# Performance work log

Hardware: AMD Instinct MI355X
Metric: run time of the kernel (lower is better)

Reference implementation:

```python
import jax, jax.numpy as jnp
import numpy as np
from jax import lax

V, E, H, C = 50000, 300, 300, 3
TP, TH, B = 128, 64, 256


def _cell(x, h, c, Wih, Whh, bih, bhh):
    # PyTorch LSTMCell: gate order i, f, g, o
    g = x @ Wih.T + bih + h @ Whh.T + bhh
    i, f, gg, o = jnp.split(g, 4, axis=-1)
    c2 = jax.nn.sigmoid(f) * c + jax.nn.sigmoid(i) * jnp.tanh(gg)
    return jax.nn.sigmoid(o) * jnp.tanh(c2), c2


def setup_inputs() -> dict:
    key = jax.random.key(0)
    ks = iter(jax.random.split(key, 32))
    def n(shape, s=0.05):
        return jax.random.normal(next(ks), shape, dtype=jnp.float32) * s
    return {
        "premise": jax.random.randint(next(ks), (TP, B), 0, V),
        "premise_len": jax.random.randint(next(ks), (B,), 1, TP),
        "hypothesis": jax.random.randint(next(ks), (TH, B), 0, V),
        "hypothesis_len": jax.random.randint(next(ks), (B,), 1, TH),
        "word2vec": n((V, E), 1.0),
        "w_e": jax.random.uniform(next(ks), (H,), dtype=jnp.float32),
        "W_s": n((H, H)), "W_t": n((H, H)), "W_m": n((H, H)),
        "fc_w": n((C, H)), "fc_b": n((C,)),
        "prem_Wih": n((4 * H, E)), "prem_Whh": n((4 * H, H)),
        "prem_bih": n((4 * H,)), "prem_bhh": n((4 * H,)),
        "hypo_Wih": n((4 * H, E)), "hypo_Whh": n((4 * H, H)),
        "hypo_bih": n((4 * H,)), "hypo_bhh": n((4 * H,)),
        "match_Wih": n((4 * H, 2 * H)), "match_Whh": n((4 * H, H)),
        "match_bih": n((4 * H,)), "match_bhh": n((4 * H,)),
    }


def reference(premise, premise_len, hypothesis, hypothesis_len, word2vec,
              w_e, W_s, W_t, W_m, fc_w, fc_b,
              prem_Wih, prem_Whh, prem_bih, prem_bhh,
              hypo_Wih, hypo_Whh, hypo_bih, hypo_bhh,
              match_Wih, match_Whh, match_bih, match_bhh):
    b = premise.shape[1]
    h = w_e.shape[0]
    prem_e = word2vec[premise]      # [TP, B, E]
    hypo_e = word2vec[hypothesis]   # [TH, B, E]
    z = jnp.zeros((b, h), dtype=word2vec.dtype)

    # premise LSTM over time
    def prem_step(carry, x):
        hs, cs = carry
        hs, cs = _cell(x, hs, cs, prem_Wih, prem_Whh, prem_bih, prem_bhh)
        return (hs, cs), hs
    _, h_s = lax.scan(prem_step, (z, z), prem_e)  # [TP, B, H]

    # precompute W_s @ h_s (invariant across hypothesis steps)
    ws_hs = jnp.einsum('tbh,kh->tbk', h_s, W_s)   # [TP, B, H]

    # hypothesis LSTM + per-step tanh attention + match cell (zero hx each step,
    # matching the original call lstm_match(m_k) with no hx)
    def hypo_step(carry, x):
        h_t, c_t, h_m = carry
        h_t, c_t = _cell(x, h_t, c_t, hypo_Wih, hypo_Whh, hypo_bih, hypo_bhh)
        q = h_t @ W_t.T + h_m @ W_m.T                   # [B, H]
        s = jnp.tanh(ws_hs + q[None])                   # [TP, B, H]
        e = jnp.einsum('tbh,h->tb', s, w_e)             # [TP, B]
        alpha = jax.nn.softmax(e, axis=0)               # softmax over premise positions
        a = jnp.einsum('tb,tbh->bh', alpha, h_s)        # [B, H]
        m = jnp.concatenate([a, h_t], axis=1)           # [B, 2H]
        h_m_new, _ = _cell(m, z, z, match_Wih, match_Whh, match_bih, match_bhh)
        return (h_t, c_t, h_m_new), None

    (_, _, h_m), _ = lax.scan(hypo_step, (z, z, z), hypo_e)
    return h_m @ fc_w.T + fc_b  # [B, C]
```

## Files before the change

kernel.cpp:

```cpp
#include <hip/hip_runtime.h>
#include <hip/hip_bf16.h>
#include <cstddef>

#define HDIM 300
#define EDIM 300
#define BATCH 256
#define TPREM 128
#define THYP 64
#define KTT 32

typedef unsigned short us8 __attribute__((ext_vector_type(8)));

__device__ __forceinline__ float fast_sigm(float x) {
    return 1.f / (1.f + __expf(-x));
}
__device__ __forceinline__ float fast_tanh(float x) {
    float e = __expf(2.f * x);
    return 1.f - 2.f / (e + 1.f);
}
__device__ __forceinline__ unsigned short f2bf(float f) {
    __hip_bfloat16 h = __float2bfloat16(f);
    return *reinterpret_cast<unsigned short*>(&h);
}
__device__ __forceinline__ float bf2f(unsigned short u) {
    return __uint_as_float((unsigned)u << 16);
}

struct Params {
    const int* premise; const int* hypothesis;
    const float* w2v; const float* w_e;
    const float* W_s; const float* W_t; const float* W_m;
    const float* fc_w; const float* fc_b;
    const float* pWih; const float* pWhh; const float* pbih; const float* pbhh;
    const float* hWih; const float* hWhh; const float* hbih; const float* hbhh;
    const float* mWih; const float* mbih; const float* mbhh;
    float* h_t_all;
    unsigned short* hsT;
    unsigned short* wshsT;
    unsigned short* wthtB;
    unsigned short* Xp;
    unsigned short* Xh;
    unsigned short* WhhW_p;
    unsigned short* WhhW_h;
    unsigned short* WmW3;
    unsigned short* WmTw;
    float* out;
};

__global__ void k_init(Params p) {
    const int stride = gridDim.x * 256;
    const int i0 = blockIdx.x * 256 + threadIdx.x;
    for (int i = i0; i < 38 * 1536 * 8; i += stride) {
        int kg = i / (1536 * 8);
        int rem = i - kg * (1536 * 8);
        int c = rem >> 3, j = rem & 7;
        int k = 8 * kg + j;
        float vp = 0.f, vh = 0.f;
        if (c < 1200 && k < 300) {
            vp = p.pWhh[(size_t)c * 300 + k];
            vh = p.hWhh[(size_t)c * 300 + k];
        }
        p.WhhW_p[i] = f2bf(vp);
        p.WhhW_h[i] = f2bf(vh);
    }
    for (int i = i0; i < 75 * 1024 * 8; i += stride) {
        int kg = i / (1024 * 8);
        int rem = i - kg * (1024 * 8);
        int c = rem >> 3, j = rem & 7;
        int k = 8 * kg + j;
        float v = 0.f;
        if (c < 900 && k < 600) {
            int row = c + (c < 300 ? 0 : 300);
            v = p.mWih[(size_t)row * 600 + k];
        }
        p.WmW3[i] = f2bf(v);
    }
    for (int i = i0; i < 38 * 304 * 8; i += stride) {
        int kg = i / (304 * 8);
        int rem = i - kg * (304 * 8);
        int c = rem >> 3, j = rem & 7;
        int k = 8 * kg + j;
        p.WmTw[i] = f2bf((c < 300 && k < 300) ? p.W_m[(size_t)c * 300 + k] : 0.f);
    }
}

__global__ __launch_bounds__(256, 2) void k_xproj(Params p) {
    __shared__ __align__(16) float As[16][136];
    __shared__ __align__(16) float Bs[16][68];
    __shared__ int toks[128];

    const int bid = blockIdx.x;
    const int mt = bid / 19, nt = bid % 19;
    const bool isP = mt < 256;
    const int m0 = (isP ? mt : mt - 256) * 128;
    const int n0 = nt * 64;
    const int* tk = isP ? p.premise : p.hypothesis;
    const float* W = isP ? p.pWih : p.hWih;
    const float* b1 = isP ? p.pbih : p.hbih;
    const float* b2 = isP ? p.pbhh : p.hbhh;
    unsigned short* X = isP ? p.Xp : p.Xh;
    const int tid = threadIdx.x;

    if (tid < 128) toks[tid] = tk[m0 + tid];
    __syncthreads();

    const int tm = tid & 15, tn = tid >> 4;
    float acc[8][4] = {};
    for (int k0 = 0; k0 < 300; k0 += 16) {
        for (int i = tid; i < 2048; i += 256) {
            int kk = i & 15, ml = i >> 4;
            int k = k0 + kk;
            As[kk][ml] = (k < 300)
                ? p.w2v[(size_t)toks[ml] * 300 + k] : 0.f;
        }
        for (int i = tid; i < 1024; i += 256) {
            int kk = i & 15, nl = i >> 4;
            int c = n0 + nl, k = k0 + kk;
            Bs[kk][nl] = (c < 1200 && k < 300)
                ? W[(size_t)c * 300 + k] : 0.f;
        }
        __syncthreads();
        #pragma unroll
        for (int kk = 0; kk < 16; ++kk) {
            float a[8], w[4];
            #pragma unroll
            for (int i = 0; i < 8; ++i) a[i] = As[kk][tm * 8 + i];
            #pragma unroll
            for (int j = 0; j < 4; ++j) w[j] = Bs[kk][tn * 4 + j];
            #pragma unroll
            for (int i = 0; i < 8; ++i)
                #pragma unroll
                for (int j = 0; j < 4; ++j)
                    acc[i][j] = fmaf(a[i], w[j], acc[i][j]);
        }
        __syncthreads();
    }
    #pragma unroll
    for (int i = 0; i < 8; ++i) {
        int rr = m0 + tm * 8 + i;
        int t = rr >> 8, b = rr & 255;
        int g = b >> 2, r = b & 3;
        size_t base = (size_t)(t * 64 + g) * 1200;
        #pragma unroll
        for (int j = 0; j < 4; ++j) {
            int c = n0 + tn * 4 + j;
            if (c < 1200)
                X[(base + c) * 4 + r] = f2bf(acc[i][j] + b1[c] + b2[c]);
        }
    }
}

__global__ __launch_bounds__(512, 2) void match_b(Params p) {
    __shared__ __align__(16) float4 A[304];
    __shared__ __align__(16) float4 G[1536];

    const int blk = blockIdx.x;
    const int tid = threadIdx.x;
    const bool isP = blk < 64;
    const int g = isP ? blk : blk - 64;
    const int b0 = g * 4;
    const int TS = isP ? TPREM : THYP;
    const unsigned short* WhhW = isP ? p.WhhW_p : p.WhhW_h;
    const unsigned short* Xbuf = isP ? p.Xp : p.Xh;

    if (tid < 304) A[tid] = {0, 0, 0, 0};
    float4 creg = {0, 0, 0, 0};
    __syncthreads();

    for (int t = 0; t < TS; ++t) {
        float4 ac0 = {0,0,0,0}, ac1 = {0,0,0,0}, ac2 = {0,0,0,0};
        {
            const unsigned short* w0 = WhhW + (size_t)tid * 8;
            const unsigned short* w1 = WhhW + (size_t)(tid + 512) * 8;
            const unsigned short* w2 = WhhW + (size_t)(tid + 1024) * 8;
            for (int kg = 0; kg < 38; kg += 2) {
                const size_t offA = (size_t)kg * (1536 * 8);
                const size_t offB = (size_t)(kg + 1) * (1536 * 8);
                us8 u0a = *reinterpret_cast<const us8*>(w0 + offA);
                us8 u1a = *reinterpret_cast<const us8*>(w1 + offA);
                us8 u2a = *reinterpret_cast<const us8*>(w2 + offA);
                us8 u0b = *reinterpret_cast<const us8*>(w0 + offB);
                us8 u1b = *reinterpret_cast<const us8*>(w1 + offB);
                us8 u2b = *reinterpret_cast<const us8*>(w2 + offB);
                #pragma unroll
                for (int j = 0; j < 8; ++j) {
                    float4 a = A[8 * kg + j];
                    float f0 = bf2f(u0a[j]), f1 = bf2f(u1a[j]), f2 = bf2f(u2a[j]);
                    ac0.x = fmaf(a.x, f0, ac0.x); ac0.y = fmaf(a.y, f0, ac0.y);
                    ac0.z = fmaf(a.z, f0, ac0.z); ac0.w = fmaf(a.w, f0, ac0.w);
                    ac1.x = fmaf(a.x, f1, ac1.x); ac1.y = fmaf(a.y, f1, ac1.y);
                    ac1.z = fmaf(a.z, f1, ac1.z); ac1.w = fmaf(a.w, f1, ac1.w);
                    ac2.x = fmaf(a.x, f2, ac2.x); ac2.y = fmaf(a.y, f2, ac2.y);
                    ac2.z = fmaf(a.z, f2, ac2.z); ac2.w = fmaf(a.w, f2, ac2.w);
                }
                #pragma unroll
                for (int j = 0; j < 8; ++j) {
                    float4 a = A[8 * (kg + 1) + j];
                    float f0 = bf2f(u0b[j]), f1 = bf2f(u1b[j]), f2 = bf2f(u2b[j]);
                    ac0.x = fmaf(a.x, f0, ac0.x); ac0.y = fmaf(a.y, f0, ac0.y);
                    ac0.z = fmaf(a.z, f0, ac0.z); ac0.w = fmaf(a.w, f0, ac0.w);
                    ac1.x = fmaf(a.x, f1, ac1.x); ac1.y = fmaf(a.y, f1, ac1.y);
                    ac1.z = fmaf(a.z, f1, ac1.z); ac1.w = fmaf(a.w, f1, ac1.w);
                    ac2.x = fmaf(a.x, f2, ac2.x); ac2.y = fmaf(a.y, f2, ac2.y);
                    ac2.z = fmaf(a.z, f2, ac2.z); ac2.w = fmaf(a.w, f2, ac2.w);
                }
            }
        }
        G[tid] = ac0;
        G[tid + 512] = ac1;
        G[tid + 1024] = ac2;
        __syncthreads();

        if (tid < 300) {
            const unsigned short* xb = Xbuf + (size_t)(t * 64 + g) * 1200 * 4;
            ushort4 xi = *reinterpret_cast<const ushort4*>(xb + (size_t)tid * 4);
            ushort4 xf = *reinterpret_cast<const ushort4*>(xb + (size_t)(tid + 300) * 4);
            ushort4 xg = *reinterpret_cast<const ushort4*>(xb + (size_t)(tid + 600) * 4);
            ushort4 xo = *reinterpret_cast<const ushort4*>(xb + (size_t)(tid + 900) * 4);
            float4 g_i = G[tid], g_f = G[300 + tid];
            float4 g_g = G[600 + tid], g_o = G[900 + tid];
            float4 h4;
            {
                float gi = fast_sigm(g_i.x + bf2f(xi.x));
                float gf = fast_sigm(g_f.x + bf2f(xf.x));
                float gg = fast_tanh(g_g.x + bf2f(xg.x));
                float go = fast_sigm(g_o.x + bf2f(xo.x));
                creg.x = gf * creg.x + gi * gg; h4.x = go * fast_tanh(creg.x);
            }
            {
                float gi = fast_sigm(g_i.y + bf2f(xi.y));
                float gf = fast_sigm(g_f.y + bf2f(xf.y));
                float gg = fast_tanh(g_g.y + bf2f(xg.y));
                float go = fast_sigm(g_o.y + bf2f(xo.y));
                creg.y = gf * creg.y + gi * gg; h4.y = go * fast_tanh(creg.y);
            }
            {
                float gi = fast_sigm(g_i.z + bf2f(xi.z));
                float gf = fast_sigm(g_f.z + bf2f(xf.z));
                float gg = fast_tanh(g_g.z + bf2f(xg.z));
                float go = fast_sigm(g_o.z + bf2f(xo.z));
                creg.z = gf * creg.z + gi * gg; h4.z = go * fast_tanh(creg.z);
            }
            {
                float gi = fast_sigm(g_i.w + bf2f(xi.w));
                float gf = fast_sigm(g_f.w + bf2f(xf.w));
                float gg = fast_tanh(g_g.w + bf2f(xg.w));
                float go = fast_sigm(g_o.w + bf2f(xo.w));
                creg.w = gf * creg.w + gi * gg; h4.w = go * fast_tanh(creg.w);
            }
            A[tid] = h4;
            if (isP) {
                p.hsT[((size_t)(b0 + 0) * TPREM + t) * HDIM + tid] = f2bf(h4.x);
                p.hsT[((size_t)(b0 + 1) * TPREM + t) * HDIM + tid] = f2bf(h4.y);
                p.hsT[((size_t)(b0 + 2) * TPREM + t) * HDIM + tid] = f2bf(h4.z);
                p.hsT[((size_t)(b0 + 3) * TPREM + t) * HDIM + tid] = f2bf(h4.w);
            } else {
                const size_t rb = (size_t)(t * BATCH + b0);
                p.h_t_all[(rb + 0) * HDIM + tid] = h4.x;
                p.h_t_all[(rb + 1) * HDIM + tid] = h4.y;
                p.h_t_all[(rb + 2) * HDIM + tid] = h4.z;
                p.h_t_all[(rb + 3) * HDIM + tid] = h4.w;
            }
        }
        __syncthreads();
    }
}

__global__ __launch_bounds__(256, 2) void k_proj(Params p) {
    __shared__ __align__(16) float hA[320][34];
    __shared__ __align__(16) float Bs[KTT][68];

    const int jb = blockIdx.x;
    const int tid = threadIdx.x;
    const int pb = tid & 15, hl = tid >> 4;
    const bool isP = jb < 1024;
    const int rt = isP ? jb : jb - 1024;
    const float* Wp = isP ? p.W_s : p.W_t;
    const int fb_c = tid >> 2, fb_k0 = (tid & 3) * 8;

    for (int i2 = tid; i2 < 32 * HDIM; i2 += 256) {
        int r = i2 / HDIM, k = i2 - r * HDIM;
        hA[k][r] = isP
            ? bf2f(p.hsT[(size_t)(rt * 32 + r) * HDIM + k])
            : p.h_t_all[(size_t)(rt * 32 + r) * HDIM + k];
    }
    for (int i2 = tid; i2 < 20 * 34; i2 += 256)
        hA[300 + i2 / 34][i2 % 34] = 0.f;
    __syncthreads();

    unsigned short* dst = isP ? p.wshsT : p.wthtB;

    for (int n0 = 0; n0 < HDIM; n0 += 64) {
        const int wrow = n0 + fb_c;
        const bool wvalid = wrow < HDIM;
        float acc[2][4] = {};
        for (int kc = 0; kc < HDIM; kc += KTT) {
            #pragma unroll
            for (int u = 0; u < 8; ++u) {
                int kk = fb_k0 + u, k = kc + kk;
                Bs[kk][fb_c] = (wvalid && k < HDIM)
                    ? Wp[(size_t)wrow * HDIM + k] : 0.f;
            }
            __syncthreads();
            #pragma unroll
            for (int kk = 0; kk < KTT; ++kk) {
                float2 av = *(const float2*)&hA[kc + kk][pb * 2];
                float4 wv = *(const float4*)&Bs[kk][hl * 4];
                acc[0][0] = fmaf(av.x, wv.x, acc[0][0]);
                acc[0][1] = fmaf(av.x, wv.y, acc[0][1]);
                acc[0][2] = fmaf(av.x, wv.z, acc[0][2]);
                acc[0][3] = fmaf(av.x, wv.w, acc[0][3]);
                acc[1][0] = fmaf(av.y, wv.x, acc[1][0]);
                acc[1][1] = fmaf(av.y, wv.y, acc[1][1]);
                acc[1][2] = fmaf(av.y, wv.z, acc[1][2]);
                acc[1][3] = fmaf(av.y, wv.w, acc[1][3]);
            }
            __syncthreads();
        }
        const int col = n0 + hl * 4;
        if (col < HDIM) {
            #pragma unroll
            for (int u = 0; u < 2; ++u) {
                size_t rr = (size_t)(rt * 32 + pb * 2 + u);
                ushort4 v4;
                v4.x = f2bf(acc[u][0]); v4.y = f2bf(acc[u][1]);
                v4.z = f2bf(acc[u][2]); v4.w = f2bf(acc[u][3]);
                *reinterpret_cast<ushort4*>(&dst[rr * HDIM + col]) = v4;
            }
        }
        __syncthreads();
    }
}

__global__ __launch_bounds__(1024, 1) void match_d(Params p) {
    __shared__ __align__(16) float hm[304];
    __shared__ __align__(16) float q[304];
    __shared__ __align__(16) float we[304];
    __shared__ float alpha[TPREM];
    __shared__ __align__(16) float A6[608];
    __shared__ float G[1024];
    __shared__ __align__(16) float pvp[16][304];

    const int b = blockIdx.x;
    const int tid = threadIdx.x;
    const int lane = tid & 63;
    const int wv = tid >> 6;
    const unsigned short* wsb = p.wshsT + (size_t)b * TPREM * HDIM;
    const unsigned short* hsb = p.hsT + (size_t)b * TPREM * HDIM;

    float bi0 = 0.f, bi2 = 0.f, bi3 = 0.f;
    if (tid < 304) { hm[tid] = 0.f; we[tid] = 0.f; q[tid] = 0.f; }
    if (tid >= 600 && tid < 608) A6[tid] = 0.f;
    if (tid < 300) {
        we[tid] = p.w_e[tid];
        bi0 = p.mbih[tid] + p.mbhh[tid];
        bi2 = p.mbih[600 + tid] + p.mbhh[600 + tid];
        bi3 = p.mbih[900 + tid] + p.mbhh[900 + tid];
    }
    __syncthreads();

    for (int k = 0; k < THYP; ++k) {
        if (tid < 304) {
            float acc = 0.f;
            const unsigned short* w0 = p.WmTw + (size_t)tid * 8;
            for (int kg = 0; kg < 38; kg += 2) {
                us8 ua = *reinterpret_cast<const us8*>(w0 + (size_t)kg * (304 * 8));
                us8 ub = *reinterpret_cast<const us8*>(w0 + (size_t)(kg + 1) * (304 * 8));
                #pragma unroll
                for (int j = 0; j < 8; ++j)
                    acc = fmaf(hm[8 * kg + j], bf2f(ua[j]), acc);
                #pragma unroll
                for (int j = 0; j < 8; ++j)
                    acc = fmaf(hm[8 * (kg + 1) + j], bf2f(ub[j]), acc);
            }
            if (tid < 300)
                q[tid] = acc + bf2f(p.wthtB[((size_t)k * BATCH + b) * HDIM + tid]);
        }
        __syncthreads();

        for (int t = wv; t < TPREM; t += 16) {
            const unsigned short* row = wsb + (size_t)t * HDIM;
            ushort4 v4 = *reinterpret_cast<const ushort4*>(&row[4 * lane]);
            float4 q4 = *reinterpret_cast<const float4*>(&q[4 * lane]);
            float4 we4 = *reinterpret_cast<const float4*>(&we[4 * lane]);
            float pp;
            pp  = we4.x * fast_tanh(bf2f(v4.x) + q4.x);
            pp += we4.y * fast_tanh(bf2f(v4.y) + q4.y);
            pp += we4.z * fast_tanh(bf2f(v4.z) + q4.z);
            pp += we4.w * fast_tanh(bf2f(v4.w) + q4.w);
            if (lane < 44) {
                int h = 256 + lane;
                pp += we[h] * fast_tanh(bf2f(row[h]) + q[h]);
            }
            #pragma unroll
            for (int off = 32; off; off >>= 1) pp += __shfl_xor(pp, off, 64);
            if (lane == 0) alpha[t] = pp;
        }
        __syncthreads();

        if (wv == 0) {
            float e0 = alpha[lane], e1 = alpha[64 + lane];
            float m = fmaxf(e0, e1);
            #pragma unroll
            for (int off = 32; off; off >>= 1) m = fmaxf(m, __shfl_xor(m, off, 64));
            e0 = __expf(e0 - m); e1 = __expf(e1 - m);
            float s = e0 + e1;
            #pragma unroll
            for (int off = 32; off; off >>= 1) s += __shfl_xor(s, off, 64);
            float inv = 1.f / s;
            alpha[lane] = e0 * inv;
            alpha[64 + lane] = e1 * inv;
        }
        __syncthreads();

        {
            float4 acc = {0, 0, 0, 0};
            float at = 0.f;
            for (int t = wv; t < TPREM; t += 16) {
                float wgt = alpha[t];
                const unsigned short* row = hsb + (size_t)t * HDIM;
                ushort4 v4 = *reinterpret_cast<const ushort4*>(&row[4 * lane]);
                acc.x = fmaf(wgt, bf2f(v4.x), acc.x);
                acc.y = fmaf(wgt, bf2f(v4.y), acc.y);
                acc.z = fmaf(wgt, bf2f(v4.z), acc.z);
                acc.w = fmaf(wgt, bf2f(v4.w), acc.w);
                if (lane < 44) at = fmaf(wgt, bf2f(row[256 + lane]), at);
            }
            *reinterpret_cast<float4*>(&pvp[wv][4 * lane]) = acc;
            if (lane < 44) pvp[wv][256 + lane] = at;
        }
        __syncthreads();

        if (tid < 300) {
            float s = 0.f;
            #pragma unroll
            for (int w16 = 0; w16 < 16; ++w16) s += pvp[w16][tid];
            A6[tid] = s;
            A6[300 + tid] = p.h_t_all[((size_t)k * BATCH + b) * HDIM + tid];
        }
        __syncthreads();

        {
            float acc0 = 0.f;
            const unsigned short* w0 = p.WmW3 + (size_t)tid * 8;
            for (int kb = 0; kb < 75; kb += 5) {
                us8 u0 = *reinterpret_cast<const us8*>(w0 + (size_t)(kb + 0) * (1024 * 8));
                us8 u1 = *reinterpret_cast<const us8*>(w0 + (size_t)(kb + 1) * (1024 * 8));
                us8 u2 = *reinterpret_cast<const us8*>(w0 + (size_t)(kb + 2) * (1024 * 8));
                us8 u3 = *reinterpret_cast<const us8*>(w0 + (size_t)(kb + 3) * (1024 * 8));
                us8 u4 = *reinterpret_cast<const us8*>(w0 + (size_t)(kb + 4) * (1024 * 8));
                #pragma unroll
                for (int j = 0; j < 8; ++j)
                    acc0 = fmaf(A6[8 * (kb + 0) + j], bf2f(u0[j]), acc0);
                #pragma unroll
                for (int j = 0; j < 8; ++j)
                    acc0 = fmaf(A6[8 * (kb + 1) + j], bf2f(u1[j]), acc0);
                #pragma unroll
                for (int j = 0; j < 8; ++j)
                    acc0 = fmaf(A6[8 * (kb + 2) + j], bf2f(u2[j]), acc0);
                #pragma unroll
                for (int j = 0; j < 8; ++j)
                    acc0 = fmaf(A6[8 * (kb + 3) + j], bf2f(u3[j]), acc0);
                #pragma unroll
                for (int j = 0; j < 8; ++j)
                    acc0 = fmaf(A6[8 * (kb + 4) + j], bf2f(u4[j]), acc0);
            }
            G[tid] = acc0;
        }
        __syncthreads();

        if (tid < 300) {
            float gi = fast_sigm(G[tid] + bi0);
            float gg = fast_tanh(G[300 + tid] + bi2);
            float go = fast_sigm(G[600 + tid] + bi3);
            hm[tid] = go * fast_tanh(gi * gg);
        }
        __syncthreads();
    }

    if (wv == 0) {
        float p0 = 0.f, p1 = 0.f, p2 = 0.f;
        #pragma unroll
        for (int i = 0; i < 5; ++i) {
            int h = lane + 64 * i;
            if (h < HDIM) {
                float v = hm[h];
                p0 = fmaf(v, p.fc_w[h], p0);
                p1 = fmaf(v, p.fc_w[HDIM + h], p1);
                p2 = fmaf(v, p.fc_w[2 * HDIM + h], p2);
            }
        }
        #pragma unroll
        for (int off = 32; off; off >>= 1) {
            p0 += __shfl_xor(p0, off, 64);
            p1 += __shfl_xor(p1, off, 64);
            p2 += __shfl_xor(p2, off, 64);
        }
        if (lane == 0) {
            p.out[b * 3 + 0] = p0 + p.fc_b[0];
            p.out[b * 3 + 1] = p1 + p.fc_b[1];
            p.out[b * 3 + 2] = p2 + p.fc_b[2];
        }
    }
}

__global__ void k_lstm_gates(
    const int* __restrict__ tok, const float* __restrict__ w2v,
    const float* __restrict__ A0, int K0,
    const float* __restrict__ A1, int K1,
    const float* __restrict__ W0, int ld0,
    const float* __restrict__ W1, int ld1,
    const float* __restrict__ bih, const float* __restrict__ bhh,
    const float* __restrict__ c_in, float* __restrict__ c_out,
    float* __restrict__ h_out)
{
    constexpr int KT = 32;
    __shared__ __align__(16) float As[KT][34];
    __shared__ __align__(16) float Bs[KT][68];

    const int tid = threadIdx.x;
    const int b0 = blockIdx.x * 32;
    const int hh0 = blockIdx.y * 16;
    const int K = K0 + K1;
    const int pb = tid & 15;
    const int hl = tid >> 4;
    const int fa_b = tid >> 3;
    const int fa_k0 = (tid & 7) * 4;
    const int fb_c = tid >> 2;
    const int fb_k0 = (tid & 3) * 8;
    const int fb_hh = hh0 + (fb_c >> 2);
    const int fb_g = fb_c & 3;
    const int fb_row = fb_g * HDIM + fb_hh;
    const bool fb_valid = fb_hh < HDIM;
    const int ga = b0 + fa_b;
    const int tok_b = tok ? tok[ga] : 0;

    float acc[2][4] = {{0.f,0.f,0.f,0.f},{0.f,0.f,0.f,0.f}};

    for (int k0 = 0; k0 < K; k0 += KT) {
        #pragma unroll
        for (int u = 0; u < 4; ++u) {
            int kk = fa_k0 + u;
            int k = k0 + kk;
            float v = 0.f;
            if (k < K0)      v = tok ? w2v[(size_t)tok_b * K0 + k]
                                     : A0[(size_t)ga * K0 + k];
            else if (k < K)  v = A1[(size_t)ga * K1 + (k - K0)];
            As[kk][fa_b] = v;
        }
        #pragma unroll
        for (int u = 0; u < 8; ++u) {
            int kk = fb_k0 + u;
            int k = k0 + kk;
            float v = 0.f;
            if (fb_valid) {
                if (k < K0)     v = W0[(size_t)fb_row * ld0 + k];
                else if (k < K) v = W1[(size_t)fb_row * ld1 + (k - K0)];
            }
            Bs[kk][fb_c] = v;
        }
        __syncthreads();
        #pragma unroll
        for (int kk = 0; kk < KT; ++kk) {
            float2 av = *(const float2*)&As[kk][pb * 2];
            float4 wv = *(const float4*)&Bs[kk][hl * 4];
            acc[0][0] = fmaf(av.x, wv.x, acc[0][0]);
            acc[0][1] = fmaf(av.x, wv.y, acc[0][1]);
            acc[0][2] = fmaf(av.x, wv.z, acc[0][2]);
            acc[0][3] = fmaf(av.x, wv.w, acc[0][3]);
            acc[1][0] = fmaf(av.y, wv.x, acc[1][0]);
            acc[1][1] = fmaf(av.y, wv.y, acc[1][1]);
            acc[1][2] = fmaf(av.y, wv.z, acc[1][2]);
            acc[1][3] = fmaf(av.y, wv.w, acc[1][3]);
        }
        __syncthreads();
    }

    const int hh = hh0 + hl;
    if (hh < HDIM) {
        float bi = bih[hh] + bhh[hh];
        float bf = bih[HDIM + hh] + bhh[HDIM + hh];
        float bg = bih[2 * HDIM + hh] + bhh[2 * HDIM + hh];
        float bo = bih[3 * HDIM + hh] + bhh[3 * HDIM + hh];
        #pragma unroll
        for (int u = 0; u < 2; ++u) {
            int b = b0 + pb * 2 + u;
            float gi = fast_sigm(acc[u][0] + bi);
            float gf = fast_sigm(acc[u][1] + bf);
            float gg = fast_tanh(acc[u][2] + bg);
            float go = fast_sigm(acc[u][3] + bo);
            float c = gf * c_in[(size_t)b * HDIM + hh] + gi * gg;
            c_out[(size_t)b * HDIM + hh] = c;
            h_out[(size_t)b * HDIM + hh] = go * fast_tanh(c);
        }
    }
}

template<int BM, int BN, int TM, int TN, int KT>
__global__ void k_gemm_tn(
    const float* __restrict__ A0, int K0,
    const float* __restrict__ A1, int K1,
    const float* __restrict__ B0, int ldb0,
    const float* __restrict__ B1, int ldb1,
    float* __restrict__ C, int M, int N)
{
    __shared__ __align__(16) float As[KT][BM + 4];
    __shared__ __align__(16) float Bs[KT][BN + 4];
    const int tid = threadIdx.x;
    const int m0 = blockIdx.x * BM;
    const int n0 = blockIdx.y * BN;
    const int K = K0 + K1;
    constexpr int TPM = BM / TM;
    const int tm = tid % TPM;
    const int tn = tid / TPM;

    float acc[TM][TN];
    #pragma unroll
    for (int i = 0; i < TM; ++i)
        #pragma unroll
        for (int j = 0; j < TN; ++j) acc[i][j] = 0.f;

    for (int k0 = 0; k0 < K; k0 += KT) {
        for (int i = tid; i < KT * BM; i += 256) {
            int kk = i % KT, ml = i / KT;
            int m = m0 + ml, k = k0 + kk;
            float v = 0.f;
            if (m < M) {
                if (k < K0)     v = A0[(size_t)m * K0 + k];
                else if (k < K) v = A1[(size_t)m * K1 + (k - K0)];
            }
            As[kk][ml] = v;
        }
        for (int i = tid; i < KT * BN; i += 256) {
            int kk = i % KT, nl = i / KT;
            int n = n0 + nl, k = k0 + kk;
            float v = 0.f;
            if (n < N) {
                if (k < K0)     v = B0[(size_t)n * ldb0 + k];
                else if (k < K) v = B1[(size_t)n * ldb1 + (k - K0)];
            }
            Bs[kk][nl] = v;
        }
        __syncthreads();
        #pragma unroll
        for (int kk = 0; kk < KT; ++kk) {
            float a[TM], w[TN];
            #pragma unroll
            for (int i = 0; i < TM; ++i) a[i] = As[kk][tm * TM + i];
            #pragma unroll
            for (int j = 0; j < TN; ++j) w[j] = Bs[kk][tn * TN + j];
            #pragma unroll
            for (int i = 0; i < TM; ++i)
                #pragma unroll
                for (int j = 0; j < TN; ++j)
                    acc[i][j] = fmaf(a[i], w[j], acc[i][j]);
        }
        __syncthreads();
    }
    #pragma unroll
    for (int i = 0; i < TM; ++i) {
        int m = m0 + tm * TM + i;
        if (m >= M) continue;
        #pragma unroll
        for (int j = 0; j < TN; ++j) {
            int n = n0 + tn * TN + j;
            if (n < N) C[(size_t)m * N + n] = acc[i][j];
        }
    }
}

__global__ void k_attn(const float* __restrict__ ws_hs,
                       const float* __restrict__ h_s,
                       const float* __restrict__ q,
                       const float* __restrict__ w_e,
                       float* __restrict__ a_out)
{
    const int b = blockIdx.x;
    const int tid = threadIdx.x;
    const int lane = tid & 63;
    const int wv = tid >> 6;

    __shared__ float q_s[HDIM];
    __shared__ float we_s[HDIM];
    __shared__ float alpha[TPREM];
    __shared__ float red[4];

    for (int h = tid; h < HDIM; h += 256) {
        q_s[h] = q[(size_t)b * HDIM + h];
        we_s[h] = w_e[h];
    }
    __syncthreads();

    for (int t = wv; t < TPREM; t += 4) {
        const float* row = ws_hs + ((size_t)t * BATCH + b) * HDIM;
        float p = 0.f;
        for (int h = lane; h < HDIM; h += 64)
            p += we_s[h] * fast_tanh(row[h] + q_s[h]);
        #pragma unroll
        for (int off = 32; off; off >>= 1) p += __shfl_xor(p, off, 64);
        if (lane == 0) alpha[t] = p;
    }
    __syncthreads();

    if (wv < 2) {
        float ev = alpha[tid];
        float m = ev;
        #pragma unroll
        for (int off = 32; off; off >>= 1) m = fmaxf(m, __shfl_xor(m, off, 64));
        if (lane == 0) red[wv] = m;
        __syncthreads();
        float gm = fmaxf(red[0], red[1]);
        float e = __expf(ev - gm);
        alpha[tid] = e;
        float s = e;
        #pragma unroll
        for (int off = 32; off; off >>= 1) s += __shfl_xor(s, off, 64);
        if (lane == 0) red[2 + wv] = s;
        __syncthreads();
        alpha[tid] *= 1.f / (red[2] + red[3]);
    } else {
        __syncthreads();
        __syncthreads();
    }
    __syncthreads();

    for (int h = tid; h < HDIM; h += 256) {
        const float* hsb = h_s + (size_t)b * HDIM + h;
        float acc = 0.f;
        #pragma unroll 4
        for (int t = 0; t < TPREM; ++t)
            acc = fmaf(alpha[t], hsb[(size_t)t * BATCH * HDIM], acc);
        a_out[(size_t)b * HDIM + h] = acc;
    }
}

__global__ void k_fc(const float* __restrict__ h_m,
                     const float* __restrict__ fc_w,
                     const float* __restrict__ fc_b,
                     float* __restrict__ out)
{
    const int b = threadIdx.x;
    float a0 = 0.f, a1 = 0.f, a2 = 0.f;
    for (int h = 0; h < HDIM; ++h) {
        float v = h_m[(size_t)b * HDIM + h];
        a0 = fmaf(v, fc_w[h], a0);
        a1 = fmaf(v, fc_w[HDIM + h], a1);
        a2 = fmaf(v, fc_w[2 * HDIM + h], a2);
    }
    out[b * 3 + 0] = a0 + fc_b[0];
    out[b * 3 + 1] = a1 + fc_b[1];
    out[b * 3 + 2] = a2 + fc_b[2];
}

extern "C" void kernel_launch(void* const* d_in, const int* in_sizes, int n_in,
                              void* d_out, int out_size, void* d_ws, size_t ws_size,
                              hipStream_t stream) {
    (void)in_sizes; (void)n_in; (void)out_size;
    const int*   premise    = (const int*)d_in[0];
    const int*   hypothesis = (const int*)d_in[2];
    const float* w2v        = (const float*)d_in[4];
    const float* w_e        = (const float*)d_in[5];
    const float* W_s        = (const float*)d_in[6];
    const float* W_t        = (const float*)d_in[7];
    const float* W_m        = (const float*)d_in[8];
    const float* fc_w       = (const float*)d_in[9];
    const float* fc_b       = (const float*)d_in[10];
    const float* pWih       = (const float*)d_in[11];
    const float* pWhh       = (const float*)d_in[12];
    const float* pbih       = (const float*)d_in[13];
    const float* pbhh       = (const float*)d_in[14];
    const float* hWih       = (const float*)d_in[15];
    const float* hWhh       = (const float*)d_in[16];
    const float* hbih       = (const float*)d_in[17];
    const float* hbhh       = (const float*)d_in[18];
    const float* mWih       = (const float*)d_in[19];
    const float* mbih       = (const float*)d_in[21];
    const float* mbhh       = (const float*)d_in[22];

    const size_t BH = (size_t)BATCH * HDIM;
    const size_t F32_CNT = (size_t)THYP * BH;
    const size_t NWHH = (size_t)38 * 1536 * 8;
    const size_t NWM3 = (size_t)75 * 1024 * 8;
    const size_t NWMT = (size_t)38 * 304 * 8;
    const size_t U16_CNT = 2 * (size_t)TPREM * BH
                         + (size_t)THYP * BH
                         + (size_t)TPREM * 64 * 1200 * 4
                         + (size_t)THYP * 64 * 1200 * 4
                         + 2 * NWHH + NWM3 + NWMT;
    const size_t NEED = F32_CNT * 4 + U16_CNT * 2 + 256;

    if (ws_size >= NEED) {
        Params p;
        p.premise = premise; p.hypothesis = hypothesis;
        p.w2v = w2v; p.w_e = w_e;
        p.W_s = W_s; p.W_t = W_t; p.W_m = W_m;
        p.fc_w = fc_w; p.fc_b = fc_b;
        p.pWih = pWih; p.pWhh = pWhh; p.pbih = pbih; p.pbhh = pbhh;
        p.hWih = hWih; p.hWhh = hWhh; p.hbih = hbih; p.hbhh = hbhh;
        p.mWih = mWih; p.mbih = mbih; p.mbhh = mbhh;

        float* f = (float*)d_ws;
        p.h_t_all = f; f += F32_CNT;
        unsigned short* u = (unsigned short*)f;
        p.hsT    = u; u += (size_t)TPREM * BH;
        p.wshsT  = u; u += (size_t)TPREM * BH;
        p.wthtB  = u; u += (size_t)THYP * BH;
        p.Xp     = u; u += (size_t)TPREM * 64 * 1200 * 4;
        p.Xh     = u; u += (size_t)THYP * 64 * 1200 * 4;
        p.WhhW_p = u; u += NWHH;
        p.WhhW_h = u; u += NWHH;
        p.WmW3   = u; u += NWM3;
        p.WmTw   = u;
        p.out = (float*)d_out;

        k_init<<<512, 256, 0, stream>>>(p);
        k_xproj<<<(256 + 128) * 19, 256, 0, stream>>>(p);
        match_b<<<128, 512, 0, stream>>>(p);
        k_proj<<<1536, 256, 0, stream>>>(p);
        match_d<<<BATCH, 1024, 0, stream>>>(p);
        return;
    }

    float* ws    = (float*)d_ws;
    float* h_s   = ws;
    float* wshs  = h_s + (size_t)TPREM * BH;
    float* zeros = wshs + (size_t)TPREM * BH;
    float* c_p   = zeros + BH;
    float* c_h   = c_p + BH;
    float* c_m   = c_h + BH;
    float* ht0   = c_m + BH;
    float* ht1   = ht0 + BH;
    float* h_m   = ht1 + BH;
    float* qb    = h_m + BH;
    float* ab    = qb + BH;

    (void)hipMemsetAsync(zeros, 0, BH * sizeof(float), stream);
    (void)hipMemsetAsync(c_p,   0, BH * sizeof(float), stream);
    (void)hipMemsetAsync(c_h,   0, BH * sizeof(float), stream);
    (void)hipMemsetAsync(h_m,   0, BH * sizeof(float), stream);

    dim3 gGate(BATCH / 32, (HDIM + 15) / 16);

    for (int t = 0; t < TPREM; ++t) {
        const float* hp = t ? (h_s + (size_t)(t - 1) * BH) : zeros;
        k_lstm_gates<<<gGate, 256, 0, stream>>>(
            premise + (size_t)t * BATCH, w2v, nullptr, EDIM,
            hp, HDIM, pWih, EDIM, pWhh, HDIM,
            pbih, pbhh, c_p, c_p, h_s + (size_t)t * BH);
    }

    k_gemm_tn<64, 64, 4, 4, 16><<<dim3(TPREM * BATCH / 64, (HDIM + 63) / 64), 256, 0, stream>>>(
        h_s, HDIM, nullptr, 0, W_s, HDIM, nullptr, 0, wshs, TPREM * BATCH, HDIM);

    for (int k = 0; k < THYP; ++k) {
        const float* hp = k ? ((k & 1) ? ht0 : ht1) : zeros;
        float* hc = (k & 1) ? ht1 : ht0;
        k_lstm_gates<<<gGate, 256, 0, stream>>>(
            hypothesis + (size_t)k * BATCH, w2v, nullptr, EDIM,
            hp, HDIM, hWih, EDIM, hWhh, HDIM,
            hbih, hbhh, c_h, c_h, hc);
        k_gemm_tn<16, 64, 1, 4, 16><<<dim3(BATCH / 16, (HDIM + 63) / 64), 256, 0, stream>>>(
            hc, HDIM, h_m, HDIM, W_t, HDIM, W_m, HDIM, qb, BATCH, HDIM);
        k_attn<<<BATCH, 256, 0, stream>>>(wshs, h_s, qb, w_e, ab);
        k_lstm_gates<<<gGate, 256, 0, stream>>>(
            nullptr, nullptr, ab, HDIM,
            hc, HDIM, mWih, 2 * HDIM, mWih + HDIM, 2 * HDIM,
            mbih, mbhh, zeros, c_m, h_m);
    }

    k_fc<<<1, BATCH, 0, stream>>>(h_m, fc_w, fc_b, (float*)d_out);
}
```

Before: 4.820 ms.

## Halve batch per block in LSTM recurrence and split-K the attention query GEMV

The premise and hypothesis LSTM recurrence kernel now processes 2 batch columns per block instead of 4, doubling the grid to 256 blocks so more CUs work on the sequential recurrence. The cost is that each block re-reads the full recurrent weight matrix, so weight traffic doubles. Separately, the per-step W_m·h_m GEMV in the match kernel is split across 912 threads in three K-chunks that are reduced through shared memory, in place of only 304 active threads. That adds an extra barrier each hypothesis step.

```diff
diff --git a/kernel.cpp b/kernel.cpp
--- a/kernel.cpp
+++ b/kernel.cpp
@@ -151,24 +151,26 @@
 }
 
 __global__ __launch_bounds__(512, 2) void match_b(Params p) {
-    __shared__ __align__(16) float4 A[304];
-    __shared__ __align__(16) float4 G[1536];
+    __shared__ __align__(16) float2 A[304];
+    __shared__ __align__(16) float2 G[1536];
 
     const int blk = blockIdx.x;
     const int tid = threadIdx.x;
-    const bool isP = blk < 64;
-    const int g = isP ? blk : blk - 64;
-    const int b0 = g * 4;
+    const bool isP = blk < 128;
+    const int g = isP ? blk : blk - 128;
+    const int b0 = g * 2;
     const int TS = isP ? TPREM : THYP;
     const unsigned short* WhhW = isP ? p.WhhW_p : p.WhhW_h;
     const unsigned short* Xbuf = isP ? p.Xp : p.Xh;
-
-    if (tid < 304) A[tid] = {0, 0, 0, 0};
-    float4 creg = {0, 0, 0, 0};
+    const int g4 = b0 >> 2;
+    const int r0 = b0 & 3;
+
+    if (tid < 304) A[tid] = {0, 0};
+    float2 creg = {0, 0};
     __syncthreads();
 
     for (int t = 0; t < TS; ++t) {
-        float4 ac0 = {0,0,0,0}, ac1 = {0,0,0,0}, ac2 = {0,0,0,0};
+        float2 ac0 = {0,0}, ac1 = {0,0}, ac2 = {0,0};
         {
             const unsigned short* w0 = WhhW + (size_t)tid * 8;
             const unsigned short* w1 = WhhW + (size_t)(tid + 512) * 8;
@@ -184,25 +186,19 @@
                 us8 u2b = *reinterpret_cast<const us8*>(w2 + offB);
                 #pragma unroll
                 for (int j = 0; j < 8; ++j) {
-                    float4 a = A[8 * kg + j];
+                    float2 a = A[8 * kg + j];
                     float f0 = bf2f(u0a[j]), f1 = bf2f(u1a[j]), f2 = bf2f(u2a[j]);
                     ac0.x = fmaf(a.x, f0, ac0.x); ac0.y = fmaf(a.y, f0, ac0.y);
-                    ac0.z = fmaf(a.z, f0, ac0.z); ac0.w = fmaf(a.w, f0, ac0.w);
                     ac1.x = fmaf(a.x, f1, ac1.x); ac1.y = fmaf(a.y, f1, ac1.y);
-                    ac1.z = fmaf(a.z, f1, ac1.z); ac1.w = fmaf(a.w, f1, ac1.w);
                     ac2.x = fmaf(a.x, f2, ac2.x); ac2.y = fmaf(a.y, f2, ac2.y);
-                    ac2.z = fmaf(a.z, f2, ac2.z); ac2.w = fmaf(a.w, f2, ac2.w);
                 }
                 #pragma unroll
                 for (int j = 0; j < 8; ++j) {
-                    float4 a = A[8 * (kg + 1) + j];
+                    float2 a = A[8 * (kg + 1) + j];
                     float f0 = bf2f(u0b[j]), f1 = bf2f(u1b[j]), f2 = bf2f(u2b[j]);
                     ac0.x = fmaf(a.x, f0, ac0.x); ac0.y = fmaf(a.y, f0, ac0.y);
-                    ac0.z = fmaf(a.z, f0, ac0.z); ac0.w = fmaf(a.w, f0, ac0.w);
                     ac1.x = fmaf(a.x, f1, ac1.x); ac1.y = fmaf(a.y, f1, ac1.y);
-                    ac1.z = fmaf(a.z, f1, ac1.z); ac1.w = fmaf(a.w, f1, ac1.w);
                     ac2.x = fmaf(a.x, f2, ac2.x); ac2.y = fmaf(a.y, f2, ac2.y);
-                    ac2.z = fmaf(a.z, f2, ac2.z); ac2.w = fmaf(a.w, f2, ac2.w);
                 }
             }
         }
@@ -212,54 +208,36 @@
         __syncthreads();
 
         if (tid < 300) {
-            const unsigned short* xb = Xbuf + (size_t)(t * 64 + g) * 1200 * 4;
-            ushort4 xi = *reinterpret_cast<const ushort4*>(xb + (size_t)tid * 4);
-            ushort4 xf = *reinterpret_cast<const ushort4*>(xb + (size_t)(tid + 300) * 4);
-            ushort4 xg = *reinterpret_cast<const ushort4*>(xb + (size_t)(tid + 600) * 4);
-            ushort4 xo = *reinterpret_cast<const ushort4*>(xb + (size_t)(tid + 900) * 4);
-            float4 g_i = G[tid], g_f = G[300 + tid];
-            float4 g_g = G[600 + tid], g_o = G[900 + tid];
-            float4 h4;
+            const unsigned short* xb = Xbuf + (size_t)(t * 64 + g4) * 1200 * 4 + r0;
+            ushort2 xi = *reinterpret_cast<const ushort2*>(xb + (size_t)tid * 4);
+            ushort2 xf = *reinterpret_cast<const ushort2*>(xb + (size_t)(tid + 300) * 4);
+            ushort2 xg = *reinterpret_cast<const ushort2*>(xb + (size_t)(tid + 600) * 4);
+            ushort2 xo = *reinterpret_cast<const ushort2*>(xb + (size_t)(tid + 900) * 4);
+            float2 g_i = G[tid], g_f = G[300 + tid];
+            float2 g_g = G[600 + tid], g_o = G[900 + tid];
+            float2 h2;
             {
                 float gi = fast_sigm(g_i.x + bf2f(xi.x));
                 float gf = fast_sigm(g_f.x + bf2f(xf.x));
                 float gg = fast_tanh(g_g.x + bf2f(xg.x));
                 float go = fast_sigm(g_o.x + bf2f(xo.x));
-                creg.x = gf * creg.x + gi * gg; h4.x = go * fast_tanh(creg.x);
+                creg.x = gf * creg.x + gi * gg; h2.x = go * fast_tanh(creg.x);
             }
             {
                 float gi = fast_sigm(g_i.y + bf2f(xi.y));
                 float gf = fast_sigm(g_f.y + bf2f(xf.y));
                 float gg = fast_tanh(g_g.y + bf2f(xg.y));
                 float go = fast_sigm(g_o.y + bf2f(xo.y));
-                creg.y = gf * creg.y + gi * gg; h4.y = go * fast_tanh(creg.y);
-            }
-            {
-                float gi = fast_sigm(g_i.z + bf2f(xi.z));
-                float gf = fast_sigm(g_f.z + bf2f(xf.z));
-                float gg = fast_tanh(g_g.z + bf2f(xg.z));
-                float go = fast_sigm(g_o.z + bf2f(xo.z));
-                creg.z = gf * creg.z + gi * gg; h4.z = go * fast_tanh(creg.z);
-            }
-            {
-                float gi = fast_sigm(g_i.w + bf2f(xi.w));
-                float gf = fast_sigm(g_f.w + bf2f(xf.w));
-                float gg = fast_tanh(g_g.w + bf2f(xg.w));
-                float go = fast_sigm(g_o.w + bf2f(xo.w));
-                creg.w = gf * creg.w + gi * gg; h4.w = go * fast_tanh(creg.w);
-            }
-            A[tid] = h4;
+                creg.y = gf * creg.y + gi * gg; h2.y = go * fast_tanh(creg.y);
+            }
+            A[tid] = h2;
             if (isP) {
-                p.hsT[((size_t)(b0 + 0) * TPREM + t) * HDIM + tid] = f2bf(h4.x);
-                p.hsT[((size_t)(b0 + 1) * TPREM + t) * HDIM + tid] = f2bf(h4.y);
-                p.hsT[((size_t)(b0 + 2) * TPREM + t) * HDIM + tid] = f2bf(h4.z);
-                p.hsT[((size_t)(b0 + 3) * TPREM + t) * HDIM + tid] = f2bf(h4.w);
+                p.hsT[((size_t)(b0 + 0) * TPREM + t) * HDIM + tid] = f2bf(h2.x);
+                p.hsT[((size_t)(b0 + 1) * TPREM + t) * HDIM + tid] = f2bf(h2.y);
             } else {
                 const size_t rb = (size_t)(t * BATCH + b0);
-                p.h_t_all[(rb + 0) * HDIM + tid] = h4.x;
-                p.h_t_all[(rb + 1) * HDIM + tid] = h4.y;
-                p.h_t_all[(rb + 2) * HDIM + tid] = h4.z;
-                p.h_t_all[(rb + 3) * HDIM + tid] = h4.w;
+                p.h_t_all[(rb + 0) * HDIM + tid] = h2.x;
+                p.h_t_all[(rb + 1) * HDIM + tid] = h2.y;
             }
         }
         __syncthreads();
@@ -340,6 +318,7 @@
     __shared__ __align__(16) float A6[608];
     __shared__ float G[1024];
     __shared__ __align__(16) float pvp[16][304];
+    __shared__ __align__(16) float qp[3][304];
 
     const int b = blockIdx.x;
     const int tid = threadIdx.x;
@@ -347,6 +326,11 @@
     const int wv = tid >> 6;
     const unsigned short* wsb = p.wshsT + (size_t)b * TPREM * HDIM;
     const unsigned short* hsb = p.hsT + (size_t)b * TPREM * HDIM;
+
+    const int qs = tid / 304;
+    const int qc = tid - qs * 304;
+    const int kg0 = (qs == 0) ? 0 : (qs == 1) ? 13 : 26;
+    const int kg1 = (qs == 0) ? 13 : (qs == 1) ? 26 : 38;
 
     float bi0 = 0.f, bi2 = 0.f, bi3 = 0.f;
     if (tid < 304) { hm[tid] = 0.f; we[tid] = 0.f; q[tid] = 0.f; }
@@ -360,22 +344,21 @@
     __syncthreads();
 
     for (int k = 0; k < THYP; ++k) {
-        if (tid < 304) {
+        if (tid < 912) {
             float acc = 0.f;
-            const unsigned short* w0 = p.WmTw + (size_t)tid * 8;
-            for (int kg = 0; kg < 38; kg += 2) {
+            const unsigned short* w0 = p.WmTw + (size_t)qc * 8;
+            for (int kg = kg0; kg < kg1; ++kg) {
                 us8 ua = *reinterpret_cast<const us8*>(w0 + (size_t)kg * (304 * 8));
-                us8 ub = *reinterpret_cast<const us8*>(w0 + (size_t)(kg + 1) * (304 * 8));
                 #pragma unroll
                 for (int j = 0; j < 8; ++j)
                     acc = fmaf(hm[8 * kg + j], bf2f(ua[j]), acc);
-                #pragma unroll
-                for (int j = 0; j < 8; ++j)
-                    acc = fmaf(hm[8 * (kg + 1) + j], bf2f(ub[j]), acc);
-            }
-            if (tid < 300)
-                q[tid] = acc + bf2f(p.wthtB[((size_t)k * BATCH + b) * HDIM + tid]);
-        }
+            }
+            qp[qs][qc] = acc;
+        }
+        __syncthreads();
+        if (tid < 300)
+            q[tid] = qp[0][tid] + qp[1][tid] + qp[2][tid]
+                   + bf2f(p.wthtB[((size_t)k * BATCH + b) * HDIM + tid]);
         __syncthreads();
 
         for (int t = wv; t < TPREM; t += 16) {
@@ -815,7 +798,7 @@
 
         k_init<<<512, 256, 0, stream>>>(p);
         k_xproj<<<(256 + 128) * 19, 256, 0, stream>>>(p);
-        match_b<<<128, 512, 0, stream>>>(p);
+        match_b<<<256, 512, 0, stream>>>(p);
         k_proj<<<1536, 256, 0, stream>>>(p);
         match_d<<<BATCH, 1024, 0, stream>>>(p);
         return;
```

Measured after the change: 5.180 ms. +7.5%, slower.
